# Optimization experiments

Hardware: AMD Instinct MI355X
Metric: run time of the kernel (lower is better)

The kernel has to match this reference:

```python
import jax, jax.numpy as jnp
import numpy as np

UP = 4
INTERVAL = 4      # coarse base interval from init
SAMP_INT = 4      # sampling_interval (fine, diagonal region)
DWID = 2          # diagonal_width
K = 3             # sample_size (AutoSample conv kernel)
Q2 = float(2 ** (INTERVAL + 2)); L2 = 2 ** (8 - INTERVAL - 2) + 1   # coarse full-space LUT: 64, 5
Q1 = float(2 ** SAMP_INT);       L1 = 2 ** (8 - SAMP_INT) + 1       # fine diagonal LUT: 16, 17
DW = 2 * DWID + 1
R1 = L1 * DW * DW * DW


def round_ste(v):
    # straight-through round, as in MuLUT's round_func
    return v + jax.lax.stop_gradient(jnp.round(v) - v)


def _msb_lsb(v, q, L):
    i = jnp.clip(jnp.floor(v / q).astype(jnp.int32), 0, L - 2)
    return i, v - i.astype(v.dtype) * q


def _simplex(f, q):
    # 4D simplex (tetrahedral) interpolation weights + vertex increments.
    # f: [..., 4] LSB fractions. Sorting descending reproduces the 24-case if/else.
    order = jnp.argsort(-f, axis=-1)
    fs = jnp.take_along_axis(f, order, axis=-1)
    w = jnp.stack([q - fs[..., 0],
                   fs[..., 0] - fs[..., 1],
                   fs[..., 1] - fs[..., 2],
                   fs[..., 2] - fs[..., 3],
                   fs[..., 3]], axis=-1) / q              # [...,5]
    oh = jax.nn.one_hot(order, 4, dtype=jnp.int32)        # [...,4,4]
    inc = jnp.cumsum(oh, axis=-2)
    inc = jnp.concatenate([jnp.zeros_like(inc[..., :1, :]), inc], axis=-2)  # [...,5,4]
    return w, inc


def _interp_mode(img, sw, w1, w2, res, r2i):
    # img [N,1,H,W] in [0,255]; sw [4,1,K,K]; w1 [R1,oc] fine LUT; w2 [L2^4,oc] coarse LUT; res [oc]
    pad = K - 1
    imgp = jnp.pad(img, ((0, 0), (0, 0), (0, pad), (0, pad)), mode='edge')
    abcd = jax.lax.conv_general_dilated(imgp, sw, (1, 1), 'VALID',
                                        dimension_numbers=('NCHW', 'OIHW', 'NCHW'))
    v = jnp.clip(jnp.moveaxis(abcd, 1, -1), 0.0, 255.0)   # [N,H,W,4] sampled (a,b,c,d)
    # coarse full-space path (compress2)
    i2, f2 = _msb_lsb(v, Q2, L2)
    wgt2, inc2 = _simplex(f2, Q2)
    vert2 = jnp.clip(i2[..., None, :] + inc2, 0, L2 - 1)  # [N,H,W,5,4]
    flat2 = ((vert2[..., 0] * L2 + vert2[..., 1]) * L2 + vert2[..., 2]) * L2 + vert2[..., 3]
    out2 = jnp.einsum('...v,...vo->...o', wgt2, w2[flat2])
    # fine diagonal path (compress1 via ref2index)
    i1, f1 = _msb_lsb(v, Q1, L1)
    wgt1, inc1 = _simplex(f1, Q1)
    vert1 = jnp.clip(i1[..., None, :] + inc1, 0, L1 - 1)
    jx = vert1[..., 0]
    off = jnp.clip(vert1[..., 1:] - jx[..., None] + DWID, 0, DW - 1)
    rows = r2i[jx, off[..., 0], off[..., 1], off[..., 2]]
    out1 = jnp.einsum('...v,...vo->...o', wgt1, w1[rows])
    within = ((jnp.abs(i1[..., 1] - i1[..., 0]) <= DWID - 1) &
              (jnp.abs(i1[..., 2] - i1[..., 0]) <= DWID - 1) &
              (jnp.abs(i1[..., 3] - i1[..., 0]) <= DWID - 1))
    return jnp.where(within[..., None], out1, out2) + res  # [N,H,W,oc]


def _stage(img, sw, w1, w2, res, r2i):
    # mode x rotation ensemble; sw [M,4,1,K,K]; w1 [M,R1,oc]; w2 [M,625,oc]; res [M,oc]
    M = sw.shape[0]
    acc = 0.0
    for m in range(M):
        for r in range(4):
            xr = jnp.rot90(img, r, axes=(2, 3))
            o = _interp_mode(xr, sw[m], w1[m], w2[m], res[m], r2i)
            o = jnp.moveaxis(o, -1, 1)                    # [N,oc,h,w]
            acc = acc + jnp.rot90(o, -r, axes=(2, 3))
    return acc / (4.0 * M)


def _stage6(feat, sw, w1, w2, res, r2i):
    # feat [N,4,H,W]; sw [M,4,4,1,K,K]; w1 [M,4,R1,up^2]; res [M,4,up^2]
    M = sw.shape[0]
    acc = 0.0
    for m in range(M):
        for c in range(4):
            for r in range(4):
                xr = jnp.rot90(feat[:, c:c + 1], r, axes=(2, 3))
                o = _interp_mode(xr, sw[m, c], w1[m, c], w2[m, c], res[m, c], r2i)
                N, h, w, _ = o.shape
                # pixel shuffle before rotating back
                o = o.reshape(N, h, w, UP, UP).transpose(0, 1, 3, 2, 4).reshape(N, 1, h * UP, w * UP)
                acc = acc + jnp.rot90(o, -r, axes=(2, 3))
    return acc / (4.0 * 4.0 * M)


def setup_inputs() -> dict:
    key = jax.random.key(0)
    ks = jax.random.split(key, 14)
    B, H, W = 2, 192, 192
    x = jax.random.uniform(ks[0], (B, 1, H, W), jnp.float32)
    ref2index = jnp.arange(R1, dtype=jnp.int64).reshape(L1, DW, DW, DW)
    # samplers scaled to keep sampled pixel values roughly in [0,255]
    samp_s123 = jax.random.uniform(ks[1], (3, 3, 4, 1, K, K), jnp.float32) / (K * K)
    samp_s4 = jax.random.uniform(ks[2], (3, 4, 1, K, K), jnp.float32) / (K * K)
    samp_s6 = jax.random.uniform(ks[3], (3, 4, 4, 1, K, K), jnp.float32) / (K * K)
    w1_s123 = jax.random.normal(ks[4], (3, 3, R1, 2), jnp.float32) * 0.1
    w2_s123 = jax.random.normal(ks[5], (3, 3, L2 ** 4, 2), jnp.float32) * 0.1
    res_s123 = jax.random.normal(ks[6], (3, 3, 2), jnp.float32) * 0.01
    w1_s4 = jax.random.normal(ks[7], (3, R1, 1), jnp.float32) * 0.1
    w2_s4 = jax.random.normal(ks[8], (3, L2 ** 4, 1), jnp.float32) * 0.1
    res_s4 = jax.random.normal(ks[9], (3, 1), jnp.float32) * 0.01
    w1_s6 = jax.random.normal(ks[10], (3, 4, R1, UP * UP), jnp.float32) * 0.1
    w2_s6 = jax.random.normal(ks[11], (3, 4, L2 ** 4, UP * UP), jnp.float32) * 0.1
    res_s6 = jax.random.normal(ks[12], (3, 4, UP * UP), jnp.float32) * 0.01
    return {'x': x, 'ref2index': ref2index,
            'samp_s123': samp_s123, 'w1_s123': w1_s123, 'w2_s123': w2_s123, 'res_s123': res_s123,
            'samp_s4': samp_s4, 'w1_s4': w1_s4, 'w2_s4': w2_s4, 'res_s4': res_s4,
            'samp_s6': samp_s6, 'w1_s6': w1_s6, 'w2_s6': w2_s6, 'res_s6': res_s6}


def reference(x, ref2index, samp_s123, w1_s123, w2_s123, res_s123,
              samp_s4, w1_s4, w2_s4, res_s4,
              samp_s6, w1_s6, w2_s6, res_s6):
    cur = round_ste(jnp.clip(x * 255.0, 0.0, 255.0))
    refine = []
    for s in range(3):  # stages 1-3, out_c=2: ch0 -> refine, ch1 -> next stage
        pred = _stage(cur, samp_s123[s], w1_s123[s], w2_s123[s], res_s123[s], ref2index)
        y = round_ste(jnp.clip(pred * 255.0, 0.0, 255.0))
        refine.append(y[:, 0:1])
        cur = y[:, 1:2]
    pred = _stage(cur, samp_s4, w1_s4, w2_s4, res_s4, ref2index)  # stage 4, out_c=1
    refine.append(round_ste(jnp.clip(pred * 255.0, 0.0, 255.0)))
    feat = jnp.concatenate(refine, axis=1)  # [B,4,H,W]
    hr = _stage6(feat, samp_s6, w1_s6, w2_s6, res_s6, ref2index)  # [B,1,H*up,W*up]
    return jnp.clip(hr * 255.0, 0.0, 255.0) / 255.0
```

## Files before the change

### kernel.cpp

```cpp
#include <hip/hip_runtime.h>

#define HW   192
#define HW2  (HW*HW)
#define NPIX (2*HW2)
#define NUP  (HW*4)

__device__ __forceinline__ float clamp255f(float v){ return fminf(fmaxf(v,0.f),255.f); }

__device__ __forceinline__ void simplex_setup(const float v4[4],
    const float* __restrict__ w1m, const float* __restrict__ w2m,
    const float*& tab, int idx[5], float wgt[5])
{
  float f1[4], f2[4]; int i1[4], i2[4];
#pragma unroll
  for (int k=0;k<4;k++){
    float vk = clamp255f(v4[k]);
    int a = (int)(vk*0.0625f);   a = a>15?15:a;
    int b = (int)(vk*0.015625f); b = b>3 ?3 :b;
    i1[k]=a; f1[k]=vk-(float)a*16.f;
    i2[k]=b; f2[k]=vk-(float)b*64.f;
  }
  const int d1=i1[1]-i1[0], d2=i1[2]-i1[0], d3=i1[3]-i1[0];
  const bool within = (d1<=1)&&(d1>=-1)&&(d2<=1)&&(d2>=-1)&&(d3<=1)&&(d3>=-1);

  float ff[4]; int ii[4];
#pragma unroll
  for (int k=0;k<4;k++){ ff[k]= within?f1[k]:f2[k]; ii[k]= within?i1[k]:i2[k]; }
  const float Q    = within?16.f:64.f;
  const float qinv = within?0.0625f:0.015625f;
  tab = within? w1m : w2m;

  const int rk0 = (ff[1]> ff[0]) + (ff[2]> ff[0]) + (ff[3]> ff[0]);
  const int rk1 = (ff[0]>=ff[1]) + (ff[2]> ff[1]) + (ff[3]> ff[1]);
  const int rk2 = (ff[0]>=ff[2]) + (ff[1]>=ff[2]) + (ff[3]> ff[2]);
  const int rk3 = (ff[0]>=ff[3]) + (ff[1]>=ff[3]) + (ff[2]>=ff[3]);

  float a0=ff[0],a1=ff[1],a2=ff[2],a3=ff[3],t;
  t=fmaxf(a0,a1); a1=fminf(a0,a1); a0=t;
  t=fmaxf(a2,a3); a3=fminf(a2,a3); a2=t;
  t=fmaxf(a0,a2); a2=fminf(a0,a2); a0=t;
  t=fmaxf(a1,a3); a3=fminf(a1,a3); a1=t;
  t=fmaxf(a1,a2); a2=fminf(a1,a2); a1=t;

  wgt[0]=(Q-a0)*qinv; wgt[1]=(a0-a1)*qinv; wgt[2]=(a1-a2)*qinv;
  wgt[3]=(a2-a3)*qinv; wgt[4]=a3*qinv;

#pragma unroll
  for (int t5=0;t5<5;t5++){
    const int c0 = rk0<t5, c1 = rk1<t5, c2 = rk2<t5, c3 = rk3<t5;
    const int A0 = ii[0]+c0;
    const int A1 = within ? (d1 + c1 - c0 + 2) : (ii[1]+c1);
    const int A2 = within ? (d2 + c2 - c0 + 2) : (ii[2]+c2);
    const int A3 = within ? (d3 + c3 - c0 + 2) : (ii[3]+c3);
    idx[t5] = A0*125 + A1*25 + A2*5 + A3;
  }
}

template<int OUTC>
__device__ __forceinline__ void interp_eval(const float v4[4],
    const float* __restrict__ w1m, const float* __restrict__ w2m, float* out)
{
  const float* tab; int idx[5]; float wgt[5];
  simplex_setup(v4, w1m, w2m, tab, idx, wgt);
  float s[OUTC];
#pragma unroll
  for (int c=0;c<OUTC;c++) s[c]=0.f;
#pragma unroll
  for (int t5=0;t5<5;t5++){
    const float w = wgt[t5];
    if constexpr (OUTC==2){
      const float2 p = reinterpret_cast<const float2*>(tab)[idx[t5]];
      s[0]=fmaf(w,p.x,s[0]); s[1]=fmaf(w,p.y,s[1]);
    } else {
      s[0]=fmaf(w, tab[idx[t5]], s[0]);
    }
  }
#pragma unroll
  for (int c=0;c<OUTC;c++) out[c]=s[c];
}

__device__ __forceinline__ void interp_accum16(const float v4[4],
    const float* __restrict__ w1m, const float* __restrict__ w2m, float acc[16])
{
  const float* tab; int idx[5]; float wgt[5];
  simplex_setup(v4, w1m, w2m, tab, idx, wgt);
#pragma unroll
  for (int t5=0;t5<5;t5++){
    const float w = wgt[t5];
    const float4* row = reinterpret_cast<const float4*>(tab + (size_t)idx[t5]*16);
    float4 p0=row[0], p1=row[1], p2=row[2], p3=row[3];
    acc[0]=fmaf(w,p0.x,acc[0]); acc[1]=fmaf(w,p0.y,acc[1]); acc[2]=fmaf(w,p0.z,acc[2]); acc[3]=fmaf(w,p0.w,acc[3]);
    acc[4]=fmaf(w,p1.x,acc[4]); acc[5]=fmaf(w,p1.y,acc[5]); acc[6]=fmaf(w,p1.z,acc[6]); acc[7]=fmaf(w,p1.w,acc[7]);
    acc[8]=fmaf(w,p2.x,acc[8]); acc[9]=fmaf(w,p2.y,acc[9]); acc[10]=fmaf(w,p2.z,acc[10]); acc[11]=fmaf(w,p2.w,acc[11]);
    acc[12]=fmaf(w,p3.x,acc[12]); acc[13]=fmaf(w,p3.y,acc[13]); acc[14]=fmaf(w,p3.z,acc[14]); acc[15]=fmaf(w,p3.w,acc[15]);
  }
}

template<int OUTC, bool QUANT>
__global__ void __launch_bounds__(256) stage_kernel(
    const float* __restrict__ img, const float* __restrict__ sw,
    const float* __restrict__ w1,  const float* __restrict__ w2,
    const float* __restrict__ res, float* __restrict__ outA, float* __restrict__ outB)
{
  const int t   = blockIdx.x*256 + threadIdx.x;
  const int r   = t & 3;
  const int m3  = (t >> 2) & 3;
  const int m   = m3 < 3 ? m3 : 2;
  const int pix = t >> 4;
  const int b = pix/HW2, rem = pix - b*HW2;
  const int y = rem/HW,  x   = rem - y*HW;
  const float* im = img + b*HW2;

  float tap[9];
#pragma unroll
  for (int kh=0;kh<3;kh++)
#pragma unroll
    for (int kw=0;kw<3;kw++){
      int ry = (r==0)? y+kh : (r==1)? y+kw : (r==2)? y-kh : y-kw;
      int cx = (r==0)? x+kw : (r==1)? x-kh : (r==2)? x-kw : x+kh;
      ry = min(max(ry,0),HW-1); cx = min(max(cx,0),HW-1);
      float p = im[ry*HW+cx];
      if constexpr (QUANT) p = rintf(clamp255f(p*255.f));
      tap[kh*3+kw]=p;
    }

  const float* swm = sw + m*36;
  float v[4];
#pragma unroll
  for (int oc=0;oc<4;oc++){
    float a=0.f;
#pragma unroll
    for (int k=0;k<9;k++) a = fmaf(swm[oc*9+k], tap[k], a);
    v[oc]=a;
  }
  float o[OUTC], pm[OUTC];
  interp_eval<OUTC>(v, w1 + (size_t)m*2125*OUTC, w2 + (size_t)m*625*OUTC, o);
#pragma unroll
  for (int c=0;c<OUTC;c++) pm[c] = o[c] + res[m*OUTC+c];

  const int lane = threadIdx.x & 63;
  const int base = lane & ~15;
  float acc[OUTC];
#pragma unroll
  for (int c=0;c<OUTC;c++) acc[c]=0.f;
#pragma unroll
  for (int j=0;j<12;j++){
#pragma unroll
    for (int c=0;c<OUTC;c++) acc[c] += __shfl(pm[c], base+j, 64);
  }

  if ((lane & 15) == 0){
    outA[pix] = rintf(clamp255f((acc[0]/12.0f)*255.0f));
    if constexpr (OUTC==2)
      outB[pix] = rintf(clamp255f((acc[1]/12.0f)*255.0f));
  }
}

__global__ void __launch_bounds__(256) stage6_kernel(
    const float* __restrict__ feat, const float* __restrict__ sw,
    const float* __restrict__ w1,   const float* __restrict__ w2,
    const float* __restrict__ res,  float* __restrict__ out)
{
  __shared__ float lds[4][64][17];
  const int lane = threadIdx.x & 63;
  const int c    = threadIdx.x >> 6;
  const int r    = lane & 3;
  const int pl   = lane >> 2;
  const int pix  = blockIdx.x*16 + pl;
  const int b  = pix/HW2, rem = pix - b*HW2;
  const int by = rem/HW,  bx  = rem - by*HW;

  const float* im = feat + (size_t)c*NPIX + b*HW2;
  float tap[9];
#pragma unroll
  for (int kh=0;kh<3;kh++)
#pragma unroll
    for (int kw=0;kw<3;kw++){
      int ry = (r==0)? by+kh : (r==1)? by+kw : (r==2)? by-kh : by-kw;
      int cx = (r==0)? bx+kw : (r==1)? bx-kh : (r==2)? bx-kw : bx+kh;
      ry = min(max(ry,0),HW-1); cx = min(max(cx,0),HW-1);
      tap[kh*3+kw] = im[ry*HW+cx];
    }

  float racc[16];
#pragma unroll
  for (int i=0;i<16;i++) racc[i]=0.f;

#pragma unroll
  for (int m=0;m<3;m++){
    const int mc = m*4 + c;
    const float* swmc = sw + mc*36;
    float v[4];
#pragma unroll
    for (int oc=0;oc<4;oc++){
      float a=0.f;
#pragma unroll
      for (int k=0;k<9;k++) a = fmaf(swmc[oc*9+k], tap[k], a);
      v[oc]=a;
    }
    const float* remc = res + mc*16;
#pragma unroll
    for (int i=0;i<16;i++) racc[i] += remc[i];
    interp_accum16(v, w1 + (size_t)mc*2125*16, w2 + (size_t)mc*625*16, racc);
  }

#pragma unroll
  for (int i=0;i<16;i++) lds[c][lane][i] = racc[i];
  __syncthreads();

  if (c == 0){
    float s[16];
#pragma unroll
    for (int i=0;i<16;i++)
      s[i] = ((lds[0][lane][i] + lds[1][lane][i]) + lds[2][lane][i]) + lds[3][lane][i];

    float po[16];
    if (r==0){
#pragma unroll
      for (int i=0;i<16;i++) po[i]=s[i];
    } else if (r==1){
#pragma unroll
      for (int p=0;p<4;p++)
#pragma unroll
        for (int q=0;q<4;q++) po[p*4+q]=s[(3-q)*4+p];
    } else if (r==2){
#pragma unroll
      for (int p=0;p<4;p++)
#pragma unroll
        for (int q=0;q<4;q++) po[p*4+q]=s[(3-p)*4+(3-q)];
    } else {
#pragma unroll
      for (int p=0;p<4;p++)
#pragma unroll
        for (int q=0;q<4;q++) po[p*4+q]=s[q*4+(3-p)];
    }

#pragma unroll
    for (int i=0;i<16;i++){
      po[i] += __shfl_xor(po[i],1);
      po[i] += __shfl_xor(po[i],2);
    }

    auto fin = [](float sv)->float{
      const float hr = sv/48.0f;
      return fminf(fmaxf(hr*255.f,0.f),255.f)/255.f;
    };
    float* op = out + (size_t)b*(NUP*NUP) + (size_t)(4*by+r)*NUP + 4*bx;
    *reinterpret_cast<float4*>(op) =
        make_float4(fin(po[r*4+0]),fin(po[r*4+1]),fin(po[r*4+2]),fin(po[r*4+3]));
  }
}

extern "C" void kernel_launch(void* const* d_in, const int* in_sizes, int n_in,
                              void* d_out, int out_size, void* d_ws, size_t ws_size,
                              hipStream_t stream)
{
  const float* x       = (const float*)d_in[0];
  const float* samp123 = (const float*)d_in[2];
  const float* w1123   = (const float*)d_in[3];
  const float* w2123   = (const float*)d_in[4];
  const float* res123  = (const float*)d_in[5];
  const float* samp4   = (const float*)d_in[6];
  const float* w14     = (const float*)d_in[7];
  const float* w24     = (const float*)d_in[8];
  const float* res4    = (const float*)d_in[9];
  const float* samp6   = (const float*)d_in[10];
  const float* w16     = (const float*)d_in[11];
  const float* w26     = (const float*)d_in[12];
  const float* res6    = (const float*)d_in[13];

  float* ws   = (float*)d_ws;
  float* feat = ws;
  float* curA = ws + 4*NPIX;
  float* curB = ws + 5*NPIX;

  const int GS = NPIX*16/256;
  const int G6 = NPIX/16;

  stage_kernel<2,true ><<<GS,256,0,stream>>>(x,    samp123,      w1123,        w2123,       res123,    feat,        curB);
  stage_kernel<2,false><<<GS,256,0,stream>>>(curB, samp123+108,  w1123+12750,  w2123+3750,  res123+6,  feat+NPIX,   curA);
  stage_kernel<2,false><<<GS,256,0,stream>>>(curA, samp123+216,  w1123+25500,  w2123+7500,  res123+12, feat+2*NPIX, curB);
  stage_kernel<1,false><<<GS,256,0,stream>>>(curB, samp4,        w14,          w24,         res4,      feat+3*NPIX, nullptr);
  stage6_kernel<<<G6,256,0,stream>>>(feat, samp6, w16, w26, res6, (float*)d_out);
}
```

Baseline: 203.4 us.

## Stage fine LUT in LDS and loop three modes per thread

The stage kernels now copy the fine diagonal LUT for all three modes into shared memory per block and read it from there, while coarse-LUT lookups still go to global memory. Each thread also handles all three sampling modes for one rotation, instead of one mode per thread, so there are 4 threads per pixel rather than 16 and the shuffle reduction shrinks. The aim is cheaper gathers and more reuse of the taps. In exchange, every block reloads up to 51KB into LDS, which costs per-block load time and limits occupancy, and registers per thread go up.

```diff
diff --git a/kernel.cpp b/kernel.cpp
--- a/kernel.cpp
+++ b/kernel.cpp
@@ -7,9 +7,8 @@
 
 __device__ __forceinline__ float clamp255f(float v){ return fminf(fmaxf(v,0.f),255.f); }
 
-__device__ __forceinline__ void simplex_setup(const float v4[4],
-    const float* __restrict__ w1m, const float* __restrict__ w2m,
-    const float*& tab, int idx[5], float wgt[5])
+__device__ __forceinline__ void simplex_core(const float v4[4],
+    bool& within_o, int idx[5], float wgt[5])
 {
   float f1[4], f2[4]; int i1[4], i2[4];
 #pragma unroll
@@ -22,13 +21,13 @@
   }
   const int d1=i1[1]-i1[0], d2=i1[2]-i1[0], d3=i1[3]-i1[0];
   const bool within = (d1<=1)&&(d1>=-1)&&(d2<=1)&&(d2>=-1)&&(d3<=1)&&(d3>=-1);
+  within_o = within;
 
   float ff[4]; int ii[4];
 #pragma unroll
   for (int k=0;k<4;k++){ ff[k]= within?f1[k]:f2[k]; ii[k]= within?i1[k]:i2[k]; }
   const float Q    = within?16.f:64.f;
   const float qinv = within?0.0625f:0.015625f;
-  tab = within? w1m : w2m;
 
   const int rk0 = (ff[1]> ff[0]) + (ff[2]> ff[0]) + (ff[3]> ff[0]);
   const int rk1 = (ff[0]>=ff[1]) + (ff[2]> ff[1]) + (ff[3]> ff[1]);
@@ -56,34 +55,12 @@
   }
 }
 
-template<int OUTC>
-__device__ __forceinline__ void interp_eval(const float v4[4],
-    const float* __restrict__ w1m, const float* __restrict__ w2m, float* out)
-{
-  const float* tab; int idx[5]; float wgt[5];
-  simplex_setup(v4, w1m, w2m, tab, idx, wgt);
-  float s[OUTC];
-#pragma unroll
-  for (int c=0;c<OUTC;c++) s[c]=0.f;
-#pragma unroll
-  for (int t5=0;t5<5;t5++){
-    const float w = wgt[t5];
-    if constexpr (OUTC==2){
-      const float2 p = reinterpret_cast<const float2*>(tab)[idx[t5]];
-      s[0]=fmaf(w,p.x,s[0]); s[1]=fmaf(w,p.y,s[1]);
-    } else {
-      s[0]=fmaf(w, tab[idx[t5]], s[0]);
-    }
-  }
-#pragma unroll
-  for (int c=0;c<OUTC;c++) out[c]=s[c];
-}
-
 __device__ __forceinline__ void interp_accum16(const float v4[4],
     const float* __restrict__ w1m, const float* __restrict__ w2m, float acc[16])
 {
-  const float* tab; int idx[5]; float wgt[5];
-  simplex_setup(v4, w1m, w2m, tab, idx, wgt);
+  bool within; int idx[5]; float wgt[5];
+  simplex_core(v4, within, idx, wgt);
+  const float* tab = within ? w1m : w2m;
 #pragma unroll
   for (int t5=0;t5<5;t5++){
     const float w = wgt[t5];
@@ -97,16 +74,18 @@
 }
 
 template<int OUTC, bool QUANT>
-__global__ void __launch_bounds__(256) stage_kernel(
+__global__ void __launch_bounds__(512) stage_kernel(
     const float* __restrict__ img, const float* __restrict__ sw,
     const float* __restrict__ w1,  const float* __restrict__ w2,
     const float* __restrict__ res, float* __restrict__ outA, float* __restrict__ outB)
 {
-  const int t   = blockIdx.x*256 + threadIdx.x;
+  __shared__ __align__(16) float lds_w1[3*2125*OUTC];
+  for (int i = threadIdx.x; i < 3*2125*OUTC; i += 512) lds_w1[i] = w1[i];
+  __syncthreads();
+
+  const int t   = blockIdx.x*512 + threadIdx.x;
   const int r   = t & 3;
-  const int m3  = (t >> 2) & 3;
-  const int m   = m3 < 3 ? m3 : 2;
-  const int pix = t >> 4;
+  const int pix = t >> 2;
   const int b = pix/HW2, rem = pix - b*HW2;
   const int y = rem/HW,  x   = rem - y*HW;
   const float* im = img + b*HW2;
@@ -124,32 +103,70 @@
       tap[kh*3+kw]=p;
     }
 
-  const float* swm = sw + m*36;
-  float v[4];
-#pragma unroll
-  for (int oc=0;oc<4;oc++){
-    float a=0.f;
-#pragma unroll
-    for (int k=0;k<9;k++) a = fmaf(swm[oc*9+k], tap[k], a);
-    v[oc]=a;
-  }
-  float o[OUTC], pm[OUTC];
-  interp_eval<OUTC>(v, w1 + (size_t)m*2125*OUTC, w2 + (size_t)m*625*OUTC, o);
-#pragma unroll
-  for (int c=0;c<OUTC;c++) pm[c] = o[c] + res[m*OUTC+c];
+  float pm[3][OUTC];
+#pragma unroll
+  for (int m=0;m<3;m++){
+    const float* swm = sw + m*36;
+    float v[4];
+#pragma unroll
+    for (int oc=0;oc<4;oc++){
+      float a=0.f;
+#pragma unroll
+      for (int k=0;k<9;k++) a = fmaf(swm[oc*9+k], tap[k], a);
+      v[oc]=a;
+    }
+
+    bool within; int idx[5]; float wgt[5];
+    simplex_core(v, within, idx, wgt);
+
+    float s[OUTC];
+#pragma unroll
+    for (int c=0;c<OUTC;c++) s[c]=0.f;
+    if constexpr (OUTC==2){
+      const float2* l2 = reinterpret_cast<const float2*>(lds_w1) + m*2125;
+      const float2* g2 = reinterpret_cast<const float2*>(w2) + m*625;
+      if (within){
+#pragma unroll
+        for (int t5=0;t5<5;t5++){
+          const float2 p = l2[idx[t5]];
+          s[0]=fmaf(wgt[t5],p.x,s[0]); s[1]=fmaf(wgt[t5],p.y,s[1]);
+        }
+      } else {
+#pragma unroll
+        for (int t5=0;t5<5;t5++){
+          const float2 p = g2[idx[t5]];
+          s[0]=fmaf(wgt[t5],p.x,s[0]); s[1]=fmaf(wgt[t5],p.y,s[1]);
+        }
+      }
+    } else {
+      const float* l1 = lds_w1 + m*2125;
+      const float* g1 = w2 + m*625;
+      if (within){
+#pragma unroll
+        for (int t5=0;t5<5;t5++) s[0]=fmaf(wgt[t5], l1[idx[t5]], s[0]);
+      } else {
+#pragma unroll
+        for (int t5=0;t5<5;t5++) s[0]=fmaf(wgt[t5], g1[idx[t5]], s[0]);
+      }
+    }
+#pragma unroll
+    for (int c=0;c<OUTC;c++) pm[m][c] = s[c] + res[m*OUTC+c];
+  }
 
   const int lane = threadIdx.x & 63;
-  const int base = lane & ~15;
+  const int base = lane & ~3;
   float acc[OUTC];
 #pragma unroll
   for (int c=0;c<OUTC;c++) acc[c]=0.f;
 #pragma unroll
-  for (int j=0;j<12;j++){
-#pragma unroll
-    for (int c=0;c<OUTC;c++) acc[c] += __shfl(pm[c], base+j, 64);
-  }
-
-  if ((lane & 15) == 0){
+  for (int m=0;m<3;m++)
+#pragma unroll
+    for (int rr=0;rr<4;rr++){
+#pragma unroll
+      for (int c=0;c<OUTC;c++) acc[c] += __shfl(pm[m][c], base+rr, 64);
+    }
+
+  if (r==0){
     outA[pix] = rintf(clamp255f((acc[0]/12.0f)*255.0f));
     if constexpr (OUTC==2)
       outB[pix] = rintf(clamp255f((acc[1]/12.0f)*255.0f));
@@ -274,12 +291,12 @@
   float* curA = ws + 4*NPIX;
   float* curB = ws + 5*NPIX;
 
-  const int GS = NPIX*16/256;
+  const int GS = NPIX*4/512;
   const int G6 = NPIX/16;
 
-  stage_kernel<2,true ><<<GS,256,0,stream>>>(x,    samp123,      w1123,        w2123,       res123,    feat,        curB);
-  stage_kernel<2,false><<<GS,256,0,stream>>>(curB, samp123+108,  w1123+12750,  w2123+3750,  res123+6,  feat+NPIX,   curA);
-  stage_kernel<2,false><<<GS,256,0,stream>>>(curA, samp123+216,  w1123+25500,  w2123+7500,  res123+12, feat+2*NPIX, curB);
-  stage_kernel<1,false><<<GS,256,0,stream>>>(curB, samp4,        w14,          w24,         res4,      feat+3*NPIX, nullptr);
+  stage_kernel<2,true ><<<GS,512,0,stream>>>(x,    samp123,      w1123,        w2123,       res123,    feat,        curB);
+  stage_kernel<2,false><<<GS,512,0,stream>>>(curB, samp123+108,  w1123+12750,  w2123+3750,  res123+6,  feat+NPIX,   curA);
+  stage_kernel<2,false><<<GS,512,0,stream>>>(curA, samp123+216,  w1123+25500,  w2123+7500,  res123+12, feat+2*NPIX, curB);
+  stage_kernel<1,false><<<GS,512,0,stream>>>(curB, samp4,        w14,          w24,         res4,      feat+3*NPIX, nullptr);
   stage6_kernel<<<G6,256,0,stream>>>(feat, samp6, w16, w26, res6, (float*)d_out);
 }
```

New measurement: 194.3 us. -4.5%, faster.

## Process all three sampling modes per thread instead of one thread per mode

Applied to the files above, without the earlier changes.

The stage kernel used 16 threads per pixel (4 rotations × 4 mode slots, one slot a duplicate), so the 3x3 tap gather was repeated and a quarter of the lanes did redundant work. Each thread now handles one rotation and loops over the three modes, reusing its gathered taps, and the grid shrinks by four. Table selection also becomes a per-load conditional instead of a selected pointer. The trade is more registers and serial work per thread in exchange for fewer wasted lanes and fewer repeated image loads.

```diff
diff --git a/kernel.cpp b/kernel.cpp
--- a/kernel.cpp
+++ b/kernel.cpp
@@ -7,9 +7,8 @@
 
 __device__ __forceinline__ float clamp255f(float v){ return fminf(fmaxf(v,0.f),255.f); }
 
-__device__ __forceinline__ void simplex_setup(const float v4[4],
-    const float* __restrict__ w1m, const float* __restrict__ w2m,
-    const float*& tab, int idx[5], float wgt[5])
+__device__ __forceinline__ void simplex_core(const float v4[4],
+    bool& within_o, int idx[5], float wgt[5])
 {
   float f1[4], f2[4]; int i1[4], i2[4];
 #pragma unroll
@@ -22,13 +21,13 @@
   }
   const int d1=i1[1]-i1[0], d2=i1[2]-i1[0], d3=i1[3]-i1[0];
   const bool within = (d1<=1)&&(d1>=-1)&&(d2<=1)&&(d2>=-1)&&(d3<=1)&&(d3>=-1);
+  within_o = within;
 
   float ff[4]; int ii[4];
 #pragma unroll
   for (int k=0;k<4;k++){ ff[k]= within?f1[k]:f2[k]; ii[k]= within?i1[k]:i2[k]; }
   const float Q    = within?16.f:64.f;
   const float qinv = within?0.0625f:0.015625f;
-  tab = within? w1m : w2m;
 
   const int rk0 = (ff[1]> ff[0]) + (ff[2]> ff[0]) + (ff[3]> ff[0]);
   const int rk1 = (ff[0]>=ff[1]) + (ff[2]> ff[1]) + (ff[3]> ff[1]);
@@ -60,8 +59,8 @@
 __device__ __forceinline__ void interp_eval(const float v4[4],
     const float* __restrict__ w1m, const float* __restrict__ w2m, float* out)
 {
-  const float* tab; int idx[5]; float wgt[5];
-  simplex_setup(v4, w1m, w2m, tab, idx, wgt);
+  bool within; int idx[5]; float wgt[5];
+  simplex_core(v4, within, idx, wgt);
   float s[OUTC];
 #pragma unroll
   for (int c=0;c<OUTC;c++) s[c]=0.f;
@@ -69,10 +68,12 @@
   for (int t5=0;t5<5;t5++){
     const float w = wgt[t5];
     if constexpr (OUTC==2){
-      const float2 p = reinterpret_cast<const float2*>(tab)[idx[t5]];
+      const float2 p = within ? reinterpret_cast<const float2*>(w1m)[idx[t5]]
+                              : reinterpret_cast<const float2*>(w2m)[idx[t5]];
       s[0]=fmaf(w,p.x,s[0]); s[1]=fmaf(w,p.y,s[1]);
     } else {
-      s[0]=fmaf(w, tab[idx[t5]], s[0]);
+      const float p = within ? w1m[idx[t5]] : w2m[idx[t5]];
+      s[0]=fmaf(w, p, s[0]);
     }
   }
 #pragma unroll
@@ -82,8 +83,9 @@
 __device__ __forceinline__ void interp_accum16(const float v4[4],
     const float* __restrict__ w1m, const float* __restrict__ w2m, float acc[16])
 {
-  const float* tab; int idx[5]; float wgt[5];
-  simplex_setup(v4, w1m, w2m, tab, idx, wgt);
+  bool within; int idx[5]; float wgt[5];
+  simplex_core(v4, within, idx, wgt);
+  const float* tab = within ? w1m : w2m;
 #pragma unroll
   for (int t5=0;t5<5;t5++){
     const float w = wgt[t5];
@@ -104,9 +106,8 @@
 {
   const int t   = blockIdx.x*256 + threadIdx.x;
   const int r   = t & 3;
-  const int m3  = (t >> 2) & 3;
-  const int m   = m3 < 3 ? m3 : 2;
-  const int pix = t >> 4;
+  const int pix = t >> 2;
+  if (pix >= NPIX) return;
   const int b = pix/HW2, rem = pix - b*HW2;
   const int y = rem/HW,  x   = rem - y*HW;
   const float* im = img + b*HW2;
@@ -124,32 +125,38 @@
       tap[kh*3+kw]=p;
     }
 
-  const float* swm = sw + m*36;
-  float v[4];
-#pragma unroll
-  for (int oc=0;oc<4;oc++){
-    float a=0.f;
-#pragma unroll
-    for (int k=0;k<9;k++) a = fmaf(swm[oc*9+k], tap[k], a);
-    v[oc]=a;
-  }
-  float o[OUTC], pm[OUTC];
-  interp_eval<OUTC>(v, w1 + (size_t)m*2125*OUTC, w2 + (size_t)m*625*OUTC, o);
-#pragma unroll
-  for (int c=0;c<OUTC;c++) pm[c] = o[c] + res[m*OUTC+c];
+  float pm[3][OUTC];
+#pragma unroll
+  for (int m=0;m<3;m++){
+    const float* swm = sw + m*36;
+    float v[4];
+#pragma unroll
+    for (int oc=0;oc<4;oc++){
+      float a=0.f;
+#pragma unroll
+      for (int k=0;k<9;k++) a = fmaf(swm[oc*9+k], tap[k], a);
+      v[oc]=a;
+    }
+    float o[OUTC];
+    interp_eval<OUTC>(v, w1 + (size_t)m*2125*OUTC, w2 + (size_t)m*625*OUTC, o);
+#pragma unroll
+    for (int c=0;c<OUTC;c++) pm[m][c] = o[c] + res[m*OUTC+c];
+  }
 
   const int lane = threadIdx.x & 63;
-  const int base = lane & ~15;
+  const int base = lane & ~3;
   float acc[OUTC];
 #pragma unroll
   for (int c=0;c<OUTC;c++) acc[c]=0.f;
 #pragma unroll
-  for (int j=0;j<12;j++){
-#pragma unroll
-    for (int c=0;c<OUTC;c++) acc[c] += __shfl(pm[c], base+j, 64);
-  }
-
-  if ((lane & 15) == 0){
+  for (int m=0;m<3;m++)
+#pragma unroll
+    for (int rr=0;rr<4;rr++){
+#pragma unroll
+      for (int c=0;c<OUTC;c++) acc[c] += __shfl(pm[m][c], base+rr, 64);
+    }
+
+  if (r==0){
     outA[pix] = rintf(clamp255f((acc[0]/12.0f)*255.0f));
     if constexpr (OUTC==2)
       outB[pix] = rintf(clamp255f((acc[1]/12.0f)*255.0f));
@@ -274,7 +281,7 @@
   float* curA = ws + 4*NPIX;
   float* curB = ws + 5*NPIX;
 
-  const int GS = NPIX*16/256;
+  const int GS = NPIX*4/256;
   const int G6 = NPIX/16;
 
   stage_kernel<2,true ><<<GS,256,0,stream>>>(x,    samp123,      w1123,        w2123,       res123,    feat,        curB);
```

New measurement: 179.2 us. -11.9%, faster.
